# Kernel tuning notes

Measured on AMD Instinct MI355X. Metric: run time of the kernel, lower is better.

Reference implementation:

```python
import jax, jax.numpy as jnp
import numpy as np

N = 65536      # nodes
E = 196608     # edges
G = 2048       # graphs
F_IN = 9
D = 128        # output_dim
H1 = 10        # heads layer 1
NEG_SLOPE = 0.2


def _gat_layer(x, src, dst, W, a_src, a_dst, bias, heads, out_c, concat):
    """PyG GATConv (add_self_loops already applied to src/dst)."""
    n = x.shape[0]
    h = (x @ W).reshape(n, heads, out_c)                     # [N,H,C]
    alpha_s = (h * a_src).sum(-1)                            # [N,H]
    alpha_d = (h * a_dst).sum(-1)                            # [N,H]
    e = jax.nn.leaky_relu(alpha_s[src] + alpha_d[dst], NEG_SLOPE)  # [E,H]
    # segment softmax over destination node
    m = jax.ops.segment_max(e, dst, num_segments=n)          # [N,H]
    ex = jnp.exp(e - m[dst])
    denom = jax.ops.segment_sum(ex, dst, num_segments=n)
    alpha = ex / (denom[dst] + 1e-16)                        # [E,H]
    out = jax.ops.segment_sum(h[src] * alpha[:, :, None], dst, num_segments=n)  # [N,H,C]
    out = out.reshape(n, heads * out_c) if concat else out.mean(1)
    return out + bias


def setup_inputs() -> dict:
    key = jax.random.key(0)
    ks = jax.random.split(key, 16)
    x = jax.random.normal(ks[0], (N, F_IN), dtype=jnp.float32)
    edge_index = jax.random.randint(ks[1], (2, E), 0, N, dtype=jnp.int64)
    edge_attr = jax.random.normal(ks[2], (E,), dtype=jnp.float32)  # unused by forward
    batch = jnp.sort(jax.random.randint(ks[3], (N,), 0, G, dtype=jnp.int64))
    s = 0.1
    params = {
        "W1": jax.random.normal(ks[4], (F_IN, H1 * D), dtype=jnp.float32) * s,
        "a_src1": jax.random.normal(ks[5], (H1, D), dtype=jnp.float32) * s,
        "a_dst1": jax.random.normal(ks[6], (H1, D), dtype=jnp.float32) * s,
        "b1": jnp.zeros((H1 * D,), dtype=jnp.float32),
        "W2": jax.random.normal(ks[7], (H1 * D, D), dtype=jnp.float32) * s,
        "a_src2": jax.random.normal(ks[8], (1, D), dtype=jnp.float32) * s,
        "a_dst2": jax.random.normal(ks[9], (1, D), dtype=jnp.float32) * s,
        "b2": jnp.zeros((D,), dtype=jnp.float32),
        "Wfc": jax.random.normal(ks[10], (D, D), dtype=jnp.float32) * s,
        "bfc": jnp.zeros((D,), dtype=jnp.float32),
    }
    return {"x": x, "edge_index": edge_index, "edge_attr": edge_attr, "batch": batch, **params}


def reference(x, edge_index, edge_attr, batch,
              W1, a_src1, a_dst1, b1, W2, a_src2, a_dst2, b2, Wfc, bfc):
    # GATConv default add_self_loops=True
    loops = jnp.arange(N, dtype=edge_index.dtype)
    src = jnp.concatenate([edge_index[0], loops])
    dst = jnp.concatenate([edge_index[1], loops])

    x1 = _gat_layer(x, src, dst, W1, a_src1, a_dst1, b1, H1, D, concat=True)
    x1 = jax.nn.elu(x1)                       # dropout = identity (eval)
    x1 = _gat_layer(x1, src, dst, W2, a_src2, a_dst2, b2, 1, D, concat=False)
    x1 = jax.nn.elu(x1)

    pooled = jax.ops.segment_max(x1, batch, num_segments=G)   # [G,D]
    pooled = jnp.where(jnp.isfinite(pooled), pooled, 0.0)      # guard empty graphs
    out = jax.nn.relu(pooled @ Wfc + bfc)
    return out
```

## Files before the change

### kernel.cpp

```cpp
#include <hip/hip_runtime.h>
#include <hip/hip_bf16.h>
#include <math.h>

#define NN 65536
#define NE 196608
#define ET (NE + NN)
#define NG 2048
#define FIN 9
#define DD 128
#define H1 10
#define KK (H1 * DD)
#define LRS 0.2f
#define XSB 36

typedef __attribute__((ext_vector_type(8))) short short8v;
typedef __attribute__((ext_vector_type(4))) float f32x4;

__device__ __forceinline__ float lrelu(float v) { return v >= 0.f ? v : LRS * v; }
__device__ __forceinline__ float eluf(float v)  { return v > 0.f ? v : expm1f(v); }

__device__ __forceinline__ unsigned short f2bf(float f) {
    unsigned int u = __float_as_uint(f);
    u += 0x7FFFu + ((u >> 16) & 1u);
    return (unsigned short)(u >> 16);
}
__device__ __forceinline__ float bf2f(unsigned short s) {
    return __uint_as_float((unsigned int)s << 16);
}

__global__ __launch_bounds__(256) void setup_kernel(
        const float* __restrict__ W1, const float* __restrict__ W2,
        const float* __restrict__ a_src1, const float* __restrict__ a_dst1,
        const float* __restrict__ x, const int* __restrict__ batch,
        unsigned short* __restrict__ W2p, unsigned short* __restrict__ W1pT,
        float* __restrict__ as1, float* __restrict__ ad1,
        int* __restrict__ deg, int* __restrict__ gptr) {
    __shared__ float ws_s[FIN * H1], wd_s[FIN * H1];
    const int b = blockIdx.x;
    const int t = threadIdx.x;
    if (b < 640) {
        int idx = b * 256 + t;
        int r  = idx & 7;
        int l  = (idx >> 3) & 63;
        int nt = (idx >> 9) & 7;
        int kt = idx >> 12;
        int k = kt * 32 + ((l >> 4) << 3) + r;
        int n = nt * 16 + (l & 15);
        W2p[idx] = f2bf(W2[(size_t)k * DD + n]);
    } else if (b < 896) {
        if (t < FIN * H1) {
            int f = t / H1, h = t - f * H1;
            float s = 0.f, d = 0.f;
            for (int c = 0; c < DD; ++c) {
                float w = W1[f * KK + h * DD + c];
                s = fmaf(w, a_src1[h * DD + c], s);
                d = fmaf(w, a_dst1[h * DD + c], d);
            }
            ws_s[t] = s;
            wd_s[t] = d;
        }
        __syncthreads();
        int n = (b - 640) * 256 + t;
        float xv[FIN];
#pragma unroll
        for (int f = 0; f < FIN; ++f) xv[f] = x[(size_t)n * FIN + f];
#pragma unroll
        for (int h = 0; h < H1; ++h) {
            float s = 0.f, d = 0.f;
#pragma unroll
            for (int f = 0; f < FIN; ++f) {
                s = fmaf(xv[f], ws_s[f * H1 + h], s);
                d = fmaf(xv[f], wd_s[f * H1 + h], d);
            }
            as1[n * H1 + h] = s;
            ad1[n * H1 + h] = d;
        }
        deg[n] = 0;
    } else if (b < 1152) {
        int n = (b - 896) * 256 + t;
        int bn = batch[n];
        int bp = (n == 0) ? -1 : batch[n - 1];
        for (int g = bp + 1; g <= bn; ++g) gptr[g] = n;
        if (n == NN - 1) {
            for (int g = bn + 1; g <= NG; ++g) gptr[g] = NN;
        }
    } else {
        int idx = (b - 1152) * 256 + t;
        int r  = idx & 7;
        int l  = (idx >> 3) & 63;
        int mt = (idx >> 9) & 7;
        int h  = idx >> 12;
        int f  = ((l >> 4) << 3) + r;
        int c  = mt * 16 + (l & 15);
        W1pT[idx] = (f < FIN) ? f2bf(W1[(size_t)f * KK + h * DD + c]) : (unsigned short)0;
    }
}

__global__ void count_kernel(const int* __restrict__ ei, int* __restrict__ deg) {
    int e = blockIdx.x * 256 + threadIdx.x;
    if (e >= ET) return;
    int d = (e < NE) ? ei[NE + e] : e - NE;
    atomicAdd(&deg[d], 1);
}

__global__ __launch_bounds__(256) void scan1_kernel(const int* __restrict__ deg,
                                                    int* __restrict__ bsum) {
    __shared__ int sc[256];
    int t = threadIdx.x, b = blockIdx.x;
    sc[t] = deg[b * 256 + t];
    __syncthreads();
    for (int off = 128; off > 0; off >>= 1) {
        if (t < off) sc[t] += sc[t + off];
        __syncthreads();
    }
    if (t == 0) bsum[b] = sc[0];
}

__global__ __launch_bounds__(256) void scan2_kernel(int* __restrict__ bsum,
                                                    int* __restrict__ rowptr) {
    __shared__ int sc[256];
    int t = threadIdx.x;
    int v = bsum[t];
    sc[t] = v;
    __syncthreads();
    for (int off = 1; off < 256; off <<= 1) {
        int u = (t >= off) ? sc[t - off] : 0;
        __syncthreads();
        sc[t] += u;
        __syncthreads();
    }
    bsum[t] = sc[t] - v;
    if (t == 255) rowptr[NN] = sc[255];
}

__global__ __launch_bounds__(256) void scan3_kernel(const int* __restrict__ deg,
                                                    const int* __restrict__ bsum,
                                                    int* __restrict__ rowptr,
                                                    int* __restrict__ cursor) {
    __shared__ int sc[256];
    int t = threadIdx.x, b = blockIdx.x;
    int i = b * 256 + t;
    int v = deg[i];
    sc[t] = v;
    __syncthreads();
    for (int off = 1; off < 256; off <<= 1) {
        int u = (t >= off) ? sc[t - off] : 0;
        __syncthreads();
        sc[t] += u;
        __syncthreads();
    }
    int r = bsum[b] + sc[t] - v;
    rowptr[i] = r;
    cursor[i] = r;
}

__global__ void scatter_kernel(const int* __restrict__ ei, int* __restrict__ cursor,
                               int* __restrict__ elist) {
    int e = blockIdx.x * 256 + threadIdx.x;
    if (e >= ET) return;
    int s, d;
    if (e < NE) { s = ei[e]; d = ei[NE + e]; } else { s = d = e - NE; }
    int pos = atomicAdd(&cursor[d], 1);
    elist[pos] = s;
}

__global__ void agg1_kernel(const int* __restrict__ rowptr, const int* __restrict__ elist,
                            const float* __restrict__ x,
                            const float* __restrict__ as1, const float* __restrict__ ad1,
                            unsigned short* __restrict__ xaggb) {
    int idx = blockIdx.x * 256 + threadIdx.x;
    if (idx >= NN * H1) return;
    int d = idx / H1, h = idx - d * H1;
    int beg = rowptr[d], end = rowptr[d + 1];
    float adh = ad1[d * H1 + h];
    float m = -INFINITY, den = 0.f;
    float xa[FIN] = {};
    for (int j = beg; j < end; ++j) {
        int s = elist[j];
        float v = lrelu(as1[s * H1 + h] + adh);
        if (v > m) {
            float sc = __expf(m - v);
            den *= sc;
#pragma unroll
            for (int f = 0; f < FIN; ++f) xa[f] *= sc;
            m = v;
        }
        float ex = __expf(v - m);
        den += ex;
        const float* xs = &x[(size_t)s * FIN];
#pragma unroll
        for (int f = 0; f < FIN; ++f) xa[f] = fmaf(ex, xs[f], xa[f]);
    }
    float inv = 1.f / (den + 1e-16f);
    unsigned int w[16];
#pragma unroll
    for (int i = 0; i < 16; ++i) w[i] = 0u;
#pragma unroll
    for (int f = 0; f < FIN; ++f) {
        unsigned int bv = f2bf(xa[f] * inv);
        w[f >> 1] |= bv << ((f & 1) * 16);
    }
    uint4* dst = (uint4*)&xaggb[(size_t)idx * 32];
    dst[0] = make_uint4(w[0], w[1], w[2], w[3]);
    dst[1] = make_uint4(w[4], w[5], w[6], w[7]);
    dst[2] = make_uint4(w[8], w[9], w[10], w[11]);
    dst[3] = make_uint4(w[12], w[13], w[14], w[15]);
}

__global__ __launch_bounds__(512, 4) void h2_gemm(
        const unsigned short* __restrict__ xaggb,
        const unsigned short* __restrict__ W1pT,
        const float* __restrict__ b1,
        const unsigned short* __restrict__ W2p,
        const float* __restrict__ a_src2, const float* __restrict__ a_dst2,
        unsigned short* __restrict__ h2b, float* __restrict__ as2,
        float* __restrict__ ad2) {
    __shared__ unsigned short Xs0[128 * 64];
    __shared__ unsigned short Xs1[128 * 64];
    __shared__ unsigned short xsb[2][128 * XSB];
    __shared__ float as_s[128], ad_s[128];
    const int t = threadIdx.x;
    const int n0 = blockIdx.x * 128;
    const int lane = t & 63;
    const int wvu = __builtin_amdgcn_readfirstlane(t >> 6);
    const int rh = wvu & 1, cq = wvu >> 1;
    const int rlo = lane & 15, khi = lane >> 4;
    const int srow = t >> 2, sseg = t & 3;

    if (t < 128) { as_s[t] = 0.f; ad_s[t] = 0.f; }

    f32x4 acc[4][2];
#pragma unroll
    for (int mt = 0; mt < 4; ++mt)
#pragma unroll
        for (int ntl = 0; ntl < 2; ++ntl)
#pragma unroll
            for (int q = 0; q < 4; ++q) acc[mt][ntl][q] = 0.f;

    *(uint4*)&xsb[0][srow * XSB + sseg * 8] =
        *(const uint4*)&xaggb[((size_t)(n0 + srow) * H1 + 0) * 32 + sseg * 8];

    for (int h = 0; h < H1; ++h) {
        const int cur = h & 1;
        __syncthreads();

        short8v a1 = *(const short8v*)&W1pT[(((size_t)h * 8 + wvu) * 64 + lane) * 8];
        float4 bv4 = *(const float4*)&b1[h * DD + wvu * 16 + khi * 4];
        unsigned short* XsW = (wvu >> 2) ? Xs1 : Xs0;
        const int gw7 = (wvu * 2 + (khi >> 1)) & 7;
#pragma unroll
        for (int nh = 0; nh < 2; ++nh) {
            f32x4 acc2[4];
#pragma unroll
            for (int j = 0; j < 4; ++j) {
                int nt = nh * 4 + j;
                short8v bfrag = *(const short8v*)&xsb[cur][(nt * 16 + rlo) * XSB + khi * 8];
                f32x4 zz = {0.f, 0.f, 0.f, 0.f};
                acc2[j] = __builtin_amdgcn_mfma_f32_16x16x32_bf16(a1, bfrag, zz, 0, 0, 0);
            }
#pragma unroll
            for (int j = 0; j < 4; ++j) {
                int nt = nh * 4 + j;
                float z0 = acc2[j][0] + bv4.x;
                float z1 = acc2[j][1] + bv4.y;
                float z2 = acc2[j][2] + bv4.z;
                float z3 = acc2[j][3] + bv4.w;
                z0 = z0 > 0.f ? z0 : __expf(z0) - 1.f;
                z1 = z1 > 0.f ? z1 : __expf(z1) - 1.f;
                z2 = z2 > 0.f ? z2 : __expf(z2) - 1.f;
                z3 = z3 > 0.f ? z3 : __expf(z3) - 1.f;
                unsigned int lo = (unsigned int)f2bf(z0) | ((unsigned int)f2bf(z1) << 16);
                unsigned int hi = (unsigned int)f2bf(z2) | ((unsigned int)f2bf(z3) << 16);
                int rown = nt * 16 + rlo;
                unsigned offu = rown * 64 + (((gw7 ^ (rown & 7)) << 3) | ((khi & 1) << 2));
                *(uint2*)&XsW[offu] = make_uint2(lo, hi);
            }
        }
        __syncthreads();

        if (h + 1 < H1) {
            *(uint4*)&xsb[cur ^ 1][srow * XSB + sseg * 8] =
                *(const uint4*)&xaggb[((size_t)(n0 + srow) * H1 + (h + 1)) * 32 + sseg * 8];
        }

#pragma unroll
        for (int ks = 0; ks < 4; ++ks) {
            const int ktabs = h * 4 + ks;
            const unsigned short* XsR = (ks >> 1) ? Xs1 : Xs0;
            const int g7 = (ks & 1) * 4 + khi;
            short8v bfr[2];
#pragma unroll
            for (int ntl = 0; ntl < 2; ++ntl) {
                const int nt = cq * 2 + ntl;
                bfr[ntl] = *(const short8v*)&W2p[(((size_t)ktabs * 8 + nt) * 64 + lane) * 8];
            }
#pragma unroll
            for (int mt = 0; mt < 4; ++mt) {
                const int row2 = rh * 64 + mt * 16 + rlo;
                unsigned offu = row2 * 64 + ((g7 ^ (row2 & 7)) << 3);
                short8v af = *(const short8v*)&XsR[offu];
                acc[mt][0] = __builtin_amdgcn_mfma_f32_16x16x32_bf16(af, bfr[0], acc[mt][0], 0, 0, 0);
                acc[mt][1] = __builtin_amdgcn_mfma_f32_16x16x32_bf16(af, bfr[1], acc[mt][1], 0, 0, 0);
            }
        }
    }

    __syncthreads();
#pragma unroll
    for (int mt = 0; mt < 4; ++mt)
#pragma unroll
        for (int ntl = 0; ntl < 2; ++ntl) {
            int col = cq * 32 + ntl * 16 + rlo;
            unsigned short* Xw = (col < 64) ? Xs0 : Xs1;
            int c64 = col & 63;
#pragma unroll
            for (int q = 0; q < 4; ++q) {
                int row = rh * 64 + mt * 16 + khi * 4 + q;
                Xw[row * 64 + c64] = f2bf(acc[mt][ntl][q]);
            }
        }
    __syncthreads();
#pragma unroll
    for (int i = 0; i < 4; ++i) {
        int j = i * 512 + t;
        int row = j >> 4;
        int c8 = (j & 15) * 8;
        const unsigned short* S = (c8 < 64) ? Xs0 : Xs1;
        uint4 v = *(const uint4*)&S[row * 64 + (c8 & 63)];
        *(uint4*)&h2b[(size_t)(n0 + row) * DD + c8] = v;
    }

    float sp[16], dp[16];
#pragma unroll
    for (int mt = 0; mt < 4; ++mt)
#pragma unroll
        for (int q = 0; q < 4; ++q) {
            float a = 0.f, b = 0.f;
#pragma unroll
            for (int ntl = 0; ntl < 2; ++ntl) {
                int col = cq * 32 + ntl * 16 + rlo;
                float v = acc[mt][ntl][q];
                a = fmaf(v, a_src2[col], a);
                b = fmaf(v, a_dst2[col], b);
            }
            sp[mt * 4 + q] = a;
            dp[mt * 4 + q] = b;
        }
#pragma unroll
    for (int off = 1; off < 16; off <<= 1) {
#pragma unroll
        for (int i = 0; i < 16; ++i) {
            sp[i] += __shfl_xor(sp[i], off);
            dp[i] += __shfl_xor(dp[i], off);
        }
    }
    if (rlo == 0) {
#pragma unroll
        for (int mt = 0; mt < 4; ++mt)
#pragma unroll
            for (int q = 0; q < 4; ++q) {
                atomicAdd(&as_s[rh * 64 + mt * 16 + khi * 4 + q], sp[mt * 4 + q]);
                atomicAdd(&ad_s[rh * 64 + mt * 16 + khi * 4 + q], dp[mt * 4 + q]);
            }
    }
    __syncthreads();
    if (t < 128) {
        as2[n0 + t] = as_s[t];
        ad2[n0 + t] = ad_s[t];
    }
}

__global__ void agg2_kernel(const int* __restrict__ rowptr, const int* __restrict__ elist,
                            const unsigned short* __restrict__ h2b,
                            const float* __restrict__ as2, const float* __restrict__ ad2,
                            const float* __restrict__ b2, unsigned short* __restrict__ x2b) {
    int gid = blockIdx.x * 256 + threadIdx.x;
    int n = gid >> 5, lane = gid & 31;
    if (n >= NN) return;
    int beg = rowptr[n], end = rowptr[n + 1];
    float adn = ad2[n];
    float m = -INFINITY, den = 0.f;
    float4 acc = make_float4(0.f, 0.f, 0.f, 0.f);
    for (int j = beg; j < end; ++j) {
        int s = elist[j];
        float v = lrelu(as2[s] + adn);
        if (v > m) {
            float sc = __expf(m - v);
            den *= sc;
            acc.x *= sc; acc.y *= sc; acc.z *= sc; acc.w *= sc;
            m = v;
        }
        float ex = __expf(v - m);
        den += ex;
        ushort4 hv = *(const ushort4*)&h2b[(size_t)s * DD + lane * 4];
        acc.x = fmaf(ex, bf2f(hv.x), acc.x);
        acc.y = fmaf(ex, bf2f(hv.y), acc.y);
        acc.z = fmaf(ex, bf2f(hv.z), acc.z);
        acc.w = fmaf(ex, bf2f(hv.w), acc.w);
    }
    float inv = 1.f / (den + 1e-16f);
    float4 bv = *(const float4*)&b2[lane * 4];
    ushort4 o;
    o.x = f2bf(eluf(acc.x * inv + bv.x));
    o.y = f2bf(eluf(acc.y * inv + bv.y));
    o.z = f2bf(eluf(acc.z * inv + bv.z));
    o.w = f2bf(eluf(acc.w * inv + bv.w));
    *(ushort4*)&x2b[(size_t)n * DD + lane * 4] = o;
}

__global__ __launch_bounds__(128) void pool_final_kernel(const int* __restrict__ gptr,
                                                         const unsigned short* __restrict__ x2b,
                                                         const float* __restrict__ Wfc,
                                                         const float* __restrict__ bfc,
                                                         float* __restrict__ out) {
    __shared__ float pl[DD];
    int g = blockIdx.x;
    int c = threadIdx.x;
    int beg = gptr[g], end = gptr[g + 1];
    float v = -INFINITY;
    for (int n = beg; n < end; ++n)
        v = fmaxf(v, bf2f(x2b[(size_t)n * DD + c]));
    if (beg == end) v = 0.f;
    pl[c] = v;
    __syncthreads();
    float acc = bfc[c];
#pragma unroll 8
    for (int k = 0; k < DD; ++k)
        acc = fmaf(pl[k], Wfc[k * DD + c], acc);
    out[(size_t)g * DD + c] = acc > 0.f ? acc : 0.f;
}

extern "C" void kernel_launch(void* const* d_in, const int* in_sizes, int n_in,
                              void* d_out, int out_size, void* d_ws, size_t ws_size,
                              hipStream_t stream) {
    const float* x      = (const float*)d_in[0];
    const int*   ei     = (const int*)d_in[1];
    const int*   batch  = (const int*)d_in[3];
    const float* W1     = (const float*)d_in[4];
    const float* a_src1 = (const float*)d_in[5];
    const float* a_dst1 = (const float*)d_in[6];
    const float* b1     = (const float*)d_in[7];
    const float* W2     = (const float*)d_in[8];
    const float* a_src2 = (const float*)d_in[9];
    const float* a_dst2 = (const float*)d_in[10];
    const float* b2     = (const float*)d_in[11];
    const float* Wfc    = (const float*)d_in[12];
    const float* bfc    = (const float*)d_in[13];
    float* out = (float*)d_out;

    float* wsf    = (float*)d_ws;
    float* as1    = wsf;
    float* ad1    = as1 + (size_t)NN * H1;
    float* as2    = ad1 + (size_t)NN * H1;
    float* ad2    = as2 + NN;
    int*   deg    = (int*)(ad2 + NN);
    int*   rowptr = deg + NN;
    int*   cursor = rowptr + NN + 1;
    int*   elist  = cursor + NN;
    int*   gptr   = elist + ET;
    int*   bsum   = gptr + NG + 1;
    size_t off = (size_t)((char*)(bsum + 256) - (char*)d_ws);
    off = (off + 15) & ~(size_t)15;
    unsigned short* W2p   = (unsigned short*)((char*)d_ws + off);
    unsigned short* W1pT  = W2p + (size_t)KK * DD;
    unsigned short* xaggb = W1pT + 40960;
    unsigned short* h2b   = xaggb + (size_t)NN * H1 * 32;
    unsigned short* x2b   = h2b + (size_t)NN * DD;

    setup_kernel     <<<1312, 256, 0, stream>>>(W1, W2, a_src1, a_dst1, x, batch,
                                                W2p, W1pT, as1, ad1, deg, gptr);
    count_kernel     <<<(ET + 255) / 256, 256, 0, stream>>>(ei, deg);
    scan1_kernel     <<<256, 256, 0, stream>>>(deg, bsum);
    scan2_kernel     <<<1, 256, 0, stream>>>(bsum, rowptr);
    scan3_kernel     <<<256, 256, 0, stream>>>(deg, bsum, rowptr, cursor);
    scatter_kernel   <<<(ET + 255) / 256, 256, 0, stream>>>(ei, cursor, elist);
    agg1_kernel      <<<(NN * H1 + 255) / 256, 256, 0, stream>>>(rowptr, elist, x, as1, ad1, xaggb);
    h2_gemm          <<<NN / 128, 512, 0, stream>>>(xaggb, W1pT, b1, W2p, a_src2, a_dst2,
                                                    h2b, as2, ad2);
    agg2_kernel      <<<(NN * 32) / 256, 256, 0, stream>>>(rowptr, elist, h2b, as2, ad2, b2, x2b);
    pool_final_kernel<<<NG, 128, 0, stream>>>(gptr, x2b, Wfc, bfc, out);
}
```

Before: 167.9 us.

## Fold degree counting into setup kernel and make agg1 one thread per node

The degree-count atomics now run as extra blocks of the setup kernel, with deg zeroed by a memset up front, which removes one kernel launch. agg1 now uses one thread per node handling all 10 heads. It does a two-pass softmax (max pass, then exp/accumulate pass) instead of an online per-head rescale, so each source's x row is loaded once rather than once per head. The cost is only 65536 threads with around 100 live accumulators each, which lowers occupancy and can spill registers, plus a second pass over the edge list.

After: 174.7 us. +4.0%, slower.

```diff
diff --git a/kernel.cpp b/kernel.cpp
--- a/kernel.cpp
+++ b/kernel.cpp
@@ -32,6 +32,7 @@
         const float* __restrict__ W1, const float* __restrict__ W2,
         const float* __restrict__ a_src1, const float* __restrict__ a_dst1,
         const float* __restrict__ x, const int* __restrict__ batch,
+        const int* __restrict__ ei,
         unsigned short* __restrict__ W2p, unsigned short* __restrict__ W1pT,
         float* __restrict__ as1, float* __restrict__ ad1,
         int* __restrict__ deg, int* __restrict__ gptr) {
@@ -75,7 +76,6 @@
             as1[n * H1 + h] = s;
             ad1[n * H1 + h] = d;
         }
-        deg[n] = 0;
     } else if (b < 1152) {
         int n = (b - 896) * 256 + t;
         int bn = batch[n];
@@ -84,7 +84,7 @@
         if (n == NN - 1) {
             for (int g = bn + 1; g <= NG; ++g) gptr[g] = NN;
         }
-    } else {
+    } else if (b < 1312) {
         int idx = (b - 1152) * 256 + t;
         int r  = idx & 7;
         int l  = (idx >> 3) & 63;
@@ -93,14 +93,13 @@
         int f  = ((l >> 4) << 3) + r;
         int c  = mt * 16 + (l & 15);
         W1pT[idx] = (f < FIN) ? f2bf(W1[(size_t)f * KK + h * DD + c]) : (unsigned short)0;
-    }
-}
-
-__global__ void count_kernel(const int* __restrict__ ei, int* __restrict__ deg) {
-    int e = blockIdx.x * 256 + threadIdx.x;
-    if (e >= ET) return;
-    int d = (e < NE) ? ei[NE + e] : e - NE;
-    atomicAdd(&deg[d], 1);
+    } else {
+        int e = (b - 1312) * 256 + t;
+        if (e < ET) {
+            int d = (e < NE) ? ei[NE + e] : e - NE;
+            atomicAdd(&deg[d], 1);
+        }
+    }
 }
 
 __global__ __launch_bounds__(256) void scan1_kernel(const int* __restrict__ deg,
@@ -164,47 +163,61 @@
     elist[pos] = s;
 }
 
-__global__ void agg1_kernel(const int* __restrict__ rowptr, const int* __restrict__ elist,
-                            const float* __restrict__ x,
-                            const float* __restrict__ as1, const float* __restrict__ ad1,
-                            unsigned short* __restrict__ xaggb) {
-    int idx = blockIdx.x * 256 + threadIdx.x;
-    if (idx >= NN * H1) return;
-    int d = idx / H1, h = idx - d * H1;
-    int beg = rowptr[d], end = rowptr[d + 1];
-    float adh = ad1[d * H1 + h];
-    float m = -INFINITY, den = 0.f;
-    float xa[FIN] = {};
+__global__ __launch_bounds__(256) void agg1_kernel(const int* __restrict__ rowptr,
+                                                   const int* __restrict__ elist,
+                                                   const float* __restrict__ x,
+                                                   const float* __restrict__ as1,
+                                                   const float* __restrict__ ad1,
+                                                   unsigned short* __restrict__ xaggb) {
+    int n = blockIdx.x * 256 + threadIdx.x;
+    if (n >= NN) return;
+    int beg = rowptr[n], end = rowptr[n + 1];
+    float adv[H1], m[H1];
+#pragma unroll
+    for (int h = 0; h < H1; ++h) {
+        adv[h] = ad1[n * H1 + h];
+        m[h] = -INFINITY;
+    }
+    for (int j = beg; j < end; ++j) {
+        const float* as = &as1[(size_t)elist[j] * H1];
+#pragma unroll
+        for (int h = 0; h < H1; ++h)
+            m[h] = fmaxf(m[h], lrelu(as[h] + adv[h]));
+    }
+    float den[H1] = {};
+    float xa[H1 * FIN] = {};
     for (int j = beg; j < end; ++j) {
         int s = elist[j];
-        float v = lrelu(as1[s * H1 + h] + adh);
-        if (v > m) {
-            float sc = __expf(m - v);
-            den *= sc;
-#pragma unroll
-            for (int f = 0; f < FIN; ++f) xa[f] *= sc;
-            m = v;
-        }
-        float ex = __expf(v - m);
-        den += ex;
-        const float* xs = &x[(size_t)s * FIN];
-#pragma unroll
-        for (int f = 0; f < FIN; ++f) xa[f] = fmaf(ex, xs[f], xa[f]);
-    }
-    float inv = 1.f / (den + 1e-16f);
-    unsigned int w[16];
-#pragma unroll
-    for (int i = 0; i < 16; ++i) w[i] = 0u;
-#pragma unroll
-    for (int f = 0; f < FIN; ++f) {
-        unsigned int bv = f2bf(xa[f] * inv);
-        w[f >> 1] |= bv << ((f & 1) * 16);
-    }
-    uint4* dst = (uint4*)&xaggb[(size_t)idx * 32];
-    dst[0] = make_uint4(w[0], w[1], w[2], w[3]);
-    dst[1] = make_uint4(w[4], w[5], w[6], w[7]);
-    dst[2] = make_uint4(w[8], w[9], w[10], w[11]);
-    dst[3] = make_uint4(w[12], w[13], w[14], w[15]);
+        const float* as = &as1[(size_t)s * H1];
+        float xs[FIN];
+#pragma unroll
+        for (int f = 0; f < FIN; ++f) xs[f] = x[(size_t)s * FIN + f];
+#pragma unroll
+        for (int h = 0; h < H1; ++h) {
+            float ex = __expf(lrelu(as[h] + adv[h]) - m[h]);
+            den[h] += ex;
+#pragma unroll
+            for (int f = 0; f < FIN; ++f)
+                xa[h * FIN + f] = fmaf(ex, xs[f], xa[h * FIN + f]);
+        }
+    }
+#pragma unroll
+    for (int h = 0; h < H1; ++h) {
+        float inv = 1.f / (den[h] + 1e-16f);
+        unsigned int w[16];
+#pragma unroll
+        for (int i = 0; i < 16; ++i) w[i] = 0u;
+#pragma unroll
+        for (int f = 0; f < FIN; ++f) {
+            unsigned int bv = f2bf(xa[h * FIN + f] * inv);
+            w[f >> 1] |= bv << ((f & 1) * 16);
+        }
+        uint4* dst = (uint4*)&xaggb[((size_t)n * H1 + h) * 32];
+        dst[0] = make_uint4(w[0], w[1], w[2], w[3]);
+        dst[1] = make_uint4(w[4], w[5], w[6], w[7]);
+        dst[2] = make_uint4(w[8], w[9], w[10], w[11]);
+        dst[3] = make_uint4(w[12], w[13], w[14], w[15]);
+    }
 }
 
 __global__ __launch_bounds__(512, 4) void h2_gemm(
@@ -467,14 +480,15 @@
     unsigned short* h2b   = xaggb + (size_t)NN * H1 * 32;
     unsigned short* x2b   = h2b + (size_t)NN * DD;
 
-    setup_kernel     <<<1312, 256, 0, stream>>>(W1, W2, a_src1, a_dst1, x, batch,
-                                                W2p, W1pT, as1, ad1, deg, gptr);
-    count_kernel     <<<(ET + 255) / 256, 256, 0, stream>>>(ei, deg);
+    hipMemsetAsync(deg, 0, (size_t)NN * sizeof(int), stream);
+    setup_kernel     <<<1312 + (ET + 255) / 256, 256, 0, stream>>>(
+                        W1, W2, a_src1, a_dst1, x, batch, ei,
+                        W2p, W1pT, as1, ad1, deg, gptr);
     scan1_kernel     <<<256, 256, 0, stream>>>(deg, bsum);
     scan2_kernel     <<<1, 256, 0, stream>>>(bsum, rowptr);
     scan3_kernel     <<<256, 256, 0, stream>>>(deg, bsum, rowptr, cursor);
     scatter_kernel   <<<(ET + 255) / 256, 256, 0, stream>>>(ei, cursor, elist);
-    agg1_kernel      <<<(NN * H1 + 255) / 256, 256, 0, stream>>>(rowptr, elist, x, as1, ad1, xaggb);
+    agg1_kernel      <<<NN / 256, 256, 0, stream>>>(rowptr, elist, x, as1, ad1, xaggb);
     h2_gemm          <<<NN / 128, 512, 0, stream>>>(xaggb, W1pT, b1, W2p, a_src2, a_dst2,
                                                     h2b, as2, ad2);
     agg2_kernel      <<<(NN * 32) / 256, 256, 0, stream>>>(rowptr, elist, h2b, as2, ad2, b2, x2b);
```

## Halve h2_gemm LDS staging and merge degree counting into setup kernel

Applied to the files above, without the earlier changes.

The per-head layer-1 output tile in h2_gemm is now produced in two 64-column halves through a single shared buffer instead of two. This halves the LDS footprint and lets the launch bound request 8 waves per SIMD instead of 4, at the cost of an extra barrier pair per head. The epilogue borrows the xsb buffer as the second half. Separately, the edge degree count moves into the setup kernel as extra blocks, and a memset zeroes deg beforehand, which removes one kernel launch.

New measurement: 249.8 us. 48.7% more time.

```diff
diff --git a/kernel.cpp b/kernel.cpp
--- a/kernel.cpp
+++ b/kernel.cpp
@@ -32,6 +32,7 @@
         const float* __restrict__ W1, const float* __restrict__ W2,
         const float* __restrict__ a_src1, const float* __restrict__ a_dst1,
         const float* __restrict__ x, const int* __restrict__ batch,
+        const int* __restrict__ ei,
         unsigned short* __restrict__ W2p, unsigned short* __restrict__ W1pT,
         float* __restrict__ as1, float* __restrict__ ad1,
         int* __restrict__ deg, int* __restrict__ gptr) {
@@ -75,7 +76,6 @@
             as1[n * H1 + h] = s;
             ad1[n * H1 + h] = d;
         }
-        deg[n] = 0;
     } else if (b < 1152) {
         int n = (b - 896) * 256 + t;
         int bn = batch[n];
@@ -84,7 +84,7 @@
         if (n == NN - 1) {
             for (int g = bn + 1; g <= NG; ++g) gptr[g] = NN;
         }
-    } else {
+    } else if (b < 1312) {
         int idx = (b - 1152) * 256 + t;
         int r  = idx & 7;
         int l  = (idx >> 3) & 63;
@@ -93,14 +93,13 @@
         int f  = ((l >> 4) << 3) + r;
         int c  = mt * 16 + (l & 15);
         W1pT[idx] = (f < FIN) ? f2bf(W1[(size_t)f * KK + h * DD + c]) : (unsigned short)0;
-    }
-}
-
-__global__ void count_kernel(const int* __restrict__ ei, int* __restrict__ deg) {
-    int e = blockIdx.x * 256 + threadIdx.x;
-    if (e >= ET) return;
-    int d = (e < NE) ? ei[NE + e] : e - NE;
-    atomicAdd(&deg[d], 1);
+    } else {
+        int e = (b - 1312) * 256 + t;
+        if (e < ET) {
+            int d = (e < NE) ? ei[NE + e] : e - NE;
+            atomicAdd(&deg[d], 1);
+        }
+    }
 }
 
 __global__ __launch_bounds__(256) void scan1_kernel(const int* __restrict__ deg,
@@ -207,7 +206,7 @@
     dst[3] = make_uint4(w[12], w[13], w[14], w[15]);
 }
 
-__global__ __launch_bounds__(512, 4) void h2_gemm(
+__global__ __launch_bounds__(512, 8) void h2_gemm(
         const unsigned short* __restrict__ xaggb,
         const unsigned short* __restrict__ W1pT,
         const float* __restrict__ b1,
@@ -215,8 +214,7 @@
         const float* __restrict__ a_src2, const float* __restrict__ a_dst2,
         unsigned short* __restrict__ h2b, float* __restrict__ as2,
         float* __restrict__ ad2) {
-    __shared__ unsigned short Xs0[128 * 64];
-    __shared__ unsigned short Xs1[128 * 64];
+    __shared__ unsigned short Xs[128 * 64];
     __shared__ unsigned short xsb[2][128 * XSB];
     __shared__ float as_s[128], ad_s[128];
     const int t = threadIdx.x;
@@ -224,6 +222,7 @@
     const int lane = t & 63;
     const int wvu = __builtin_amdgcn_readfirstlane(t >> 6);
     const int rh = wvu & 1, cq = wvu >> 1;
+    const int ct = wvu & 3, nh2 = wvu >> 2;
     const int rlo = lane & 15, khi = lane >> 4;
     const int srow = t >> 2, sseg = t & 3;
 
@@ -242,25 +241,25 @@
 
     for (int h = 0; h < H1; ++h) {
         const int cur = h & 1;
-        __syncthreads();
-
-        short8v a1 = *(const short8v*)&W1pT[(((size_t)h * 8 + wvu) * 64 + lane) * 8];
-        float4 bv4 = *(const float4*)&b1[h * DD + wvu * 16 + khi * 4];
-        unsigned short* XsW = (wvu >> 2) ? Xs1 : Xs0;
-        const int gw7 = (wvu * 2 + (khi >> 1)) & 7;
-#pragma unroll
-        for (int nh = 0; nh < 2; ++nh) {
+#pragma unroll
+        for (int half = 0; half < 2; ++half) {
+            __syncthreads();
+
+            short8v a1 = *(const short8v*)
+                &W1pT[(((size_t)h * 8 + half * 4 + ct) * 64 + lane) * 8];
+            float4 bv4 = *(const float4*)&b1[h * DD + half * 64 + ct * 16 + khi * 4];
+            const int gw7 = ct * 2 + (khi >> 1);
             f32x4 acc2[4];
 #pragma unroll
             for (int j = 0; j < 4; ++j) {
-                int nt = nh * 4 + j;
+                int nt = nh2 * 4 + j;
                 short8v bfrag = *(const short8v*)&xsb[cur][(nt * 16 + rlo) * XSB + khi * 8];
                 f32x4 zz = {0.f, 0.f, 0.f, 0.f};
                 acc2[j] = __builtin_amdgcn_mfma_f32_16x16x32_bf16(a1, bfrag, zz, 0, 0, 0);
             }
 #pragma unroll
             for (int j = 0; j < 4; ++j) {
-                int nt = nh * 4 + j;
+                int nt = nh2 * 4 + j;
                 float z0 = acc2[j][0] + bv4.x;
                 float z1 = acc2[j][1] + bv4.y;
                 float z2 = acc2[j][2] + bv4.z;
@@ -273,45 +272,45 @@
                 unsigned int hi = (unsigned int)f2bf(z2) | ((unsigned int)f2bf(z3) << 16);
                 int rown = nt * 16 + rlo;
                 unsigned offu = rown * 64 + (((gw7 ^ (rown & 7)) << 3) | ((khi & 1) << 2));
-                *(uint2*)&XsW[offu] = make_uint2(lo, hi);
-            }
-        }
-        __syncthreads();
-
-        if (h + 1 < H1) {
-            *(uint4*)&xsb[cur ^ 1][srow * XSB + sseg * 8] =
-                *(const uint4*)&xaggb[((size_t)(n0 + srow) * H1 + (h + 1)) * 32 + sseg * 8];
-        }
-
-#pragma unroll
-        for (int ks = 0; ks < 4; ++ks) {
-            const int ktabs = h * 4 + ks;
-            const unsigned short* XsR = (ks >> 1) ? Xs1 : Xs0;
-            const int g7 = (ks & 1) * 4 + khi;
-            short8v bfr[2];
-#pragma unroll
-            for (int ntl = 0; ntl < 2; ++ntl) {
-                const int nt = cq * 2 + ntl;
-                bfr[ntl] = *(const short8v*)&W2p[(((size_t)ktabs * 8 + nt) * 64 + lane) * 8];
-            }
-#pragma unroll
-            for (int mt = 0; mt < 4; ++mt) {
-                const int row2 = rh * 64 + mt * 16 + rlo;
-                unsigned offu = row2 * 64 + ((g7 ^ (row2 & 7)) << 3);
-                short8v af = *(const short8v*)&XsR[offu];
-                acc[mt][0] = __builtin_amdgcn_mfma_f32_16x16x32_bf16(af, bfr[0], acc[mt][0], 0, 0, 0);
-                acc[mt][1] = __builtin_amdgcn_mfma_f32_16x16x32_bf16(af, bfr[1], acc[mt][1], 0, 0, 0);
-            }
-        }
-    }
-
-    __syncthreads();
+                *(uint2*)&Xs[offu] = make_uint2(lo, hi);
+            }
+            __syncthreads();
+
+            if (half == 0 && h + 1 < H1) {
+                *(uint4*)&xsb[cur ^ 1][srow * XSB + sseg * 8] =
+                    *(const uint4*)&xaggb[((size_t)(n0 + srow) * H1 + (h + 1)) * 32 + sseg * 8];
+            }
+
+#pragma unroll
+            for (int ks2 = 0; ks2 < 2; ++ks2) {
+                const int ktabs = h * 4 + half * 2 + ks2;
+                const int g7 = ks2 * 4 + khi;
+                short8v bfr[2];
+#pragma unroll
+                for (int ntl = 0; ntl < 2; ++ntl) {
+                    const int nt = cq * 2 + ntl;
+                    bfr[ntl] = *(const short8v*)&W2p[(((size_t)ktabs * 8 + nt) * 64 + lane) * 8];
+                }
+#pragma unroll
+                for (int mt = 0; mt < 4; ++mt) {
+                    const int row2 = rh * 64 + mt * 16 + rlo;
+                    unsigned offu = row2 * 64 + ((g7 ^ (row2 & 7)) << 3);
+                    short8v af = *(const short8v*)&Xs[offu];
+                    acc[mt][0] = __builtin_amdgcn_mfma_f32_16x16x32_bf16(af, bfr[0], acc[mt][0], 0, 0, 0);
+                    acc[mt][1] = __builtin_amdgcn_mfma_f32_16x16x32_bf16(af, bfr[1], acc[mt][1], 0, 0, 0);
+                }
+            }
+        }
+    }
+
+    __syncthreads();
+    unsigned short* xsbf = &xsb[0][0];
 #pragma unroll
     for (int mt = 0; mt < 4; ++mt)
 #pragma unroll
         for (int ntl = 0; ntl < 2; ++ntl) {
             int col = cq * 32 + ntl * 16 + rlo;
-            unsigned short* Xw = (col < 64) ? Xs0 : Xs1;
+            unsigned short* Xw = (col < 64) ? Xs : xsbf;
             int c64 = col & 63;
 #pragma unroll
             for (int q = 0; q < 4; ++q) {
@@ -325,7 +324,7 @@
         int j = i * 512 + t;
         int row = j >> 4;
         int c8 = (j & 15) * 8;
-        const unsigned short* S = (c8 < 64) ? Xs0 : Xs1;
+        const unsigned short* S = (c8 < 64) ? Xs : xsbf;
         uint4 v = *(const uint4*)&S[row * 64 + (c8 & 63)];
         *(uint4*)&h2b[(size_t)(n0 + row) * DD + c8] = v;
     }
@@ -467,9 +466,10 @@
     unsigned short* h2b   = xaggb + (size_t)NN * H1 * 32;
     unsigned short* x2b   = h2b + (size_t)NN * DD;
 
-    setup_kernel     <<<1312, 256, 0, stream>>>(W1, W2, a_src1, a_dst1, x, batch,
-                                                W2p, W1pT, as1, ad1, deg, gptr);
-    count_kernel     <<<(ET + 255) / 256, 256, 0, stream>>>(ei, deg);
+    hipMemsetAsync(deg, 0, (size_t)NN * sizeof(int), stream);
+    setup_kernel     <<<1312 + (ET + 255) / 256, 256, 0, stream>>>(
+                        W1, W2, a_src1, a_dst1, x, batch, ei,
+                        W2p, W1pT, as1, ad1, deg, gptr);
     scan1_kernel     <<<256, 256, 0, stream>>>(deg, bsum);
     scan2_kernel     <<<1, 256, 0, stream>>>(bsum, rowptr);
     scan3_kernel     <<<256, 256, 0, stream>>>(deg, bsum, rowptr, cursor);
```
